# Performance work log

Hardware: AMD Instinct MI355X
Metric: run time of the kernel (lower is better)

Reference implementation:

```python
import jax, jax.numpy as jnp
import numpy as np

N, C, H, W = 2, 32, 56, 56   # batch, in_channels, spatial
O = 64                        # out_channels
PAD = 1                       # ConstantPad2d padding


def _shift(a, dh, dw):
    """Zero-padded shift: out[..., i, j] = a[..., i+dh, j+dw] (out of range -> 0)."""
    nd = a.ndim
    if dh:
        a = jnp.pad(a[..., dh:, :], [(0, 0)] * (nd - 2) + [(0, dh), (0, 0)])
    if dw:
        a = jnp.pad(a[..., :, dw:], [(0, 0)] * (nd - 2) + [(0, 0), (0, dw)])
    return a


def setup_inputs() -> dict:
    key = jax.random.key(0)
    k1, k2, k3 = jax.random.split(key, 3)
    x = jax.random.normal(k1, (N, C, H, W), dtype=jnp.float32)
    # weight entries are used as divisors in extract_param_p; keep them bounded
    # away from zero (magnitude in [0.5, 1.5], random sign) for a stable baseline.
    mag = jax.random.uniform(k2, (O, C, 3, 3), minval=0.5, maxval=1.5, dtype=jnp.float32)
    sgn = jnp.where(jax.random.bernoulli(k3, 0.5, (O, C, 3, 3)), 1.0, -1.0).astype(jnp.float32)
    return {"x": x, "weight": mag * sgn}


def reference(x, weight):
    w = weight  # [O, C, 3, 3]
    # --- extract predict filter P = [p0, p1, p2, p3], each [O, C] ---
    p0 = -w[:, :, 2, 0] / w[:, :, 2, 1]
    p1 = -w[:, :, 0, 2] / w[:, :, 1, 2]
    p2 = (1.0 - w[:, :, 0, 0]
          + w[:, :, 2, 0] * w[:, :, 0, 1] / w[:, :, 2, 1]
          + w[:, :, 0, 2] * w[:, :, 1, 0] / w[:, :, 1, 2]) / w[:, :, 1, 1]
    p3 = -w[:, :, 2, 2] / w[:, :, 1, 1]
    # --- extract update filter U = [u0..u4], each [O, C] ---
    u0, u1, u2, u3, u4 = (w[:, :, 0, 1], w[:, :, 2, 1],
                          w[:, :, 1, 0], w[:, :, 1, 2], w[:, :, 1, 1])

    def bc(c):  # [O, C] -> broadcastable over [N, O, C, Hp, Wp]
        return c[None, :, :, None, None]

    # forward: ConstantPad2d then vanilla lifting scheme (aux_index = 2).
    xp = jnp.pad(x, ((0, 0), (0, 0), (PAD, PAD), (PAD, PAD)))  # [N, C, Hp, Wp]
    x5 = xp[:, None, :, :, :]                                  # [N, 1, C, Hp, Wp]

    x0 = x5
    x1 = _shift(x5, 0, 1)
    x2 = _shift(x5, 1, 0)
    x3 = _shift(x5, 1, 1)
    x0_2 = _shift(x5, 2, 2)

    # predict steps (broadcast to [N, O, C, Hp, Wp])
    x1 = x1 - bc(p0) * x0
    x2 = x2 - bc(p1) * x0
    x3 = x3 - bc(p2) * x0 - bc(p3) * x0_2

    x1_2 = _shift(x1, 2, 0)
    x2_2 = _shift(x2, 0, 2)

    # update steps
    out = (x0
           + bc(u0) * x1 + bc(u1) * x1_2
           + bc(u2) * x2 + bc(u3) * x2_2
           + bc(u4) * x3)

    # crop aux_index=2 border, then sum over in_channels (channel_split loop
    # processes contiguous O slices and concatenates -> identical to full O).
    return out[:, :, :, :-2, :-2].sum(axis=2)  # [N, O, H, W]
```

## Files before the change

### kernel.cpp

```cpp
#include <hip/hip_runtime.h>


namespace {
constexpr int Nn = 2, Cc = 32, Hh = 56, Ww = 56, Oo = 64;

__global__ __launch_bounds__(256)
void lifting_conv_kernel(const float* __restrict__ x,
                         const float* __restrict__ w,
                         float* __restrict__ out)
{
    __shared__ float xs[Cc * 4 * 60];
    __shared__ float ws[8 * Cc * 12];

    const int tid = threadIdx.x;
    const int og  = blockIdx.x;
    const int ip  = blockIdx.y;
    const int n   = blockIdx.z;
    const int i0  = ip * 2;
    const int o0  = og * 8;

    for (int e = tid; e < Cc * 4 * 58; e += 256) {
        const int c   = e / (4 * 58);
        const int rem = e - c * (4 * 58);
        const int r   = rem / 58;
        const int jj  = rem - r * 58;
        const int h   = i0 - 1 + r;
        const int ws_ = jj - 1;
        float v = 0.0f;
        if ((unsigned)h < (unsigned)Hh && (unsigned)ws_ < (unsigned)Ww)
            v = x[((n * Cc + c) * Hh + h) * Ww + ws_];
        xs[(c * 4 + r) * 60 + jj] = v;
    }
    for (int e = tid; e < 8 * Cc * 9; e += 256) {
        const int o   = e / (Cc * 9);
        const int rem = e - o * (Cc * 9);
        const int c   = rem / 9;
        const int k   = rem - c * 9;
        ws[(o * Cc + c) * 12 + k] = w[((o0 + o) * Cc + c) * 9 + k];
    }
    __syncthreads();

    const int lane = tid & 63;
    const int wv   = tid >> 6;
    if (lane >= 56) return;
    const int rsub = (lane >= 28) ? 1 : 0;
    const int cp   = lane - rsub * 28;
    const int col0 = cp * 2;

    float a00 = 0.f, a01 = 0.f, a10 = 0.f, a11 = 0.f;
    const float* xbase = &xs[rsub * 60 + col0];
    const float* wb0   = &ws[(wv * 2 + 0) * (Cc * 12)];
    const float* wb1   = &ws[(wv * 2 + 1) * (Cc * 12)];

    #pragma unroll 4
    for (int c = 0; c < Cc; ++c) {
        const float* xr = xbase + c * 240;
        const float2 r0a = *(const float2*)(xr);
        const float2 r0b = *(const float2*)(xr + 2);
        const float2 r1a = *(const float2*)(xr + 60);
        const float2 r1b = *(const float2*)(xr + 62);
        const float2 r2a = *(const float2*)(xr + 120);
        const float2 r2b = *(const float2*)(xr + 122);

        const float4 wA0 = *(const float4*)(wb0 + c * 12);
        const float4 wB0 = *(const float4*)(wb0 + c * 12 + 4);
        const float  wC0 = wb0[c * 12 + 8];
        a00 += wA0.x * r0a.x + wA0.y * r0a.y + wA0.z * r0b.x
             + wA0.w * r1a.x + wB0.x * r1a.y + wB0.y * r1b.x
             + wB0.z * r2a.x + wB0.w * r2a.y + wC0  * r2b.x;
        a01 += wA0.x * r0a.y + wA0.y * r0b.x + wA0.z * r0b.y
             + wA0.w * r1a.y + wB0.x * r1b.x + wB0.y * r1b.y
             + wB0.z * r2a.y + wB0.w * r2b.x + wC0  * r2b.y;

        const float4 wA1 = *(const float4*)(wb1 + c * 12);
        const float4 wB1 = *(const float4*)(wb1 + c * 12 + 4);
        const float  wC1 = wb1[c * 12 + 8];
        a10 += wA1.x * r0a.x + wA1.y * r0a.y + wA1.z * r0b.x
             + wA1.w * r1a.x + wB1.x * r1a.y + wB1.y * r1b.x
             + wB1.z * r2a.x + wB1.w * r2a.y + wC1  * r2b.x;
        a11 += wA1.x * r0a.y + wA1.y * r0b.x + wA1.z * r0b.y
             + wA1.w * r1a.y + wB1.x * r1b.x + wB1.y * r1b.y
             + wB1.z * r2a.y + wB1.w * r2b.x + wC1  * r2b.y;
    }

    const int row = i0 + rsub;
    const int ob0 = ((n * Oo + o0 + wv * 2 + 0) * Hh + row) * Ww + col0;
    const int ob1 = ob0 + Hh * Ww;
    float2 v0; v0.x = a00; v0.y = a01;
    float2 v1; v1.x = a10; v1.y = a11;
    *(float2*)(out + ob0) = v0;
    *(float2*)(out + ob1) = v1;
}
}

extern "C" void kernel_launch(void* const* d_in, const int* in_sizes, int n_in,
                              void* d_out, int out_size, void* d_ws, size_t ws_size,
                              hipStream_t stream)
{
    const float* x = (const float*)d_in[0];
    const float* w = (const float*)d_in[1];
    float* out = (float*)d_out;

    dim3 grid(8, 28, 2);
    lifting_conv_kernel<<<grid, 256, 0, stream>>>(x, w, out);
}
```

Measured before the change: 76.47 us.

## Read weights as wave-uniform scalar loads and compute four outputs per thread

Drops the shared-memory weight staging and reads weights straight from global memory through a wave-uniform base (readfirstlane), so they can go through scalar loads. Each wave now computes 4 output channels instead of 2, which halves the grid and doubles the reuse of each staged input tile. In exchange there are fewer blocks (224 versus 448) to spread across CUs, and more scalar-load latency in the channel loop.

After: 74.33 us. 1.03x faster.

```diff
diff --git a/kernel.cpp b/kernel.cpp
--- a/kernel.cpp
+++ b/kernel.cpp
@@ -2,7 +2,7 @@
 
 
 namespace {
-constexpr int Nn = 2, Cc = 32, Hh = 56, Ww = 56, Oo = 64;
+constexpr int Cc = 32, Hh = 56, Ww = 56, Oo = 64;
 
 __global__ __launch_bounds__(256)
 void lifting_conv_kernel(const float* __restrict__ x,
@@ -10,14 +10,12 @@
                          float* __restrict__ out)
 {
     __shared__ float xs[Cc * 4 * 60];
-    __shared__ float ws[8 * Cc * 12];
 
     const int tid = threadIdx.x;
     const int og  = blockIdx.x;
     const int ip  = blockIdx.y;
     const int n   = blockIdx.z;
     const int i0  = ip * 2;
-    const int o0  = og * 8;
 
     for (int e = tid; e < Cc * 4 * 58; e += 256) {
         const int c   = e / (4 * 58);
@@ -25,18 +23,11 @@
         const int r   = rem / 58;
         const int jj  = rem - r * 58;
         const int h   = i0 - 1 + r;
-        const int ws_ = jj - 1;
+        const int col = jj - 1;
         float v = 0.0f;
-        if ((unsigned)h < (unsigned)Hh && (unsigned)ws_ < (unsigned)Ww)
-            v = x[((n * Cc + c) * Hh + h) * Ww + ws_];
+        if ((unsigned)h < (unsigned)Hh && (unsigned)col < (unsigned)Ww)
+            v = x[((n * Cc + c) * Hh + h) * Ww + col];
         xs[(c * 4 + r) * 60 + jj] = v;
-    }
-    for (int e = tid; e < 8 * Cc * 9; e += 256) {
-        const int o   = e / (Cc * 9);
-        const int rem = e - o * (Cc * 9);
-        const int c   = rem / 9;
-        const int k   = rem - c * 9;
-        ws[(o * Cc + c) * 12 + k] = w[((o0 + o) * Cc + c) * 9 + k];
     }
     __syncthreads();
 
@@ -47,12 +38,16 @@
     const int cp   = lane - rsub * 28;
     const int col0 = cp * 2;
 
-    float a00 = 0.f, a01 = 0.f, a10 = 0.f, a11 = 0.f;
+    const int o_base = __builtin_amdgcn_readfirstlane(og * 16 + wv * 4);
+    const float* __restrict__ wb = w + (size_t)o_base * Cc * 9;
+
+    float acc[4][2];
+    #pragma unroll
+    for (int i = 0; i < 4; ++i) { acc[i][0] = 0.f; acc[i][1] = 0.f; }
+
     const float* xbase = &xs[rsub * 60 + col0];
-    const float* wb0   = &ws[(wv * 2 + 0) * (Cc * 12)];
-    const float* wb1   = &ws[(wv * 2 + 1) * (Cc * 12)];
 
-    #pragma unroll 4
+    #pragma unroll 2
     for (int c = 0; c < Cc; ++c) {
         const float* xr = xbase + c * 240;
         const float2 r0a = *(const float2*)(xr);
@@ -62,34 +57,27 @@
         const float2 r2a = *(const float2*)(xr + 120);
         const float2 r2b = *(const float2*)(xr + 122);
 
-        const float4 wA0 = *(const float4*)(wb0 + c * 12);
-        const float4 wB0 = *(const float4*)(wb0 + c * 12 + 4);
-        const float  wC0 = wb0[c * 12 + 8];
-        a00 += wA0.x * r0a.x + wA0.y * r0a.y + wA0.z * r0b.x
-             + wA0.w * r1a.x + wB0.x * r1a.y + wB0.y * r1b.x
-             + wB0.z * r2a.x + wB0.w * r2a.y + wC0  * r2b.x;
-        a01 += wA0.x * r0a.y + wA0.y * r0b.x + wA0.z * r0b.y
-             + wA0.w * r1a.y + wB0.x * r1b.x + wB0.y * r1b.y
-             + wB0.z * r2a.y + wB0.w * r2b.x + wC0  * r2b.y;
-
-        const float4 wA1 = *(const float4*)(wb1 + c * 12);
-        const float4 wB1 = *(const float4*)(wb1 + c * 12 + 4);
-        const float  wC1 = wb1[c * 12 + 8];
-        a10 += wA1.x * r0a.x + wA1.y * r0a.y + wA1.z * r0b.x
-             + wA1.w * r1a.x + wB1.x * r1a.y + wB1.y * r1b.x
-             + wB1.z * r2a.x + wB1.w * r2a.y + wC1  * r2b.x;
-        a11 += wA1.x * r0a.y + wA1.y * r0b.x + wA1.z * r0b.y
-             + wA1.w * r1a.y + wB1.x * r1b.x + wB1.y * r1b.y
-             + wB1.z * r2a.y + wB1.w * r2b.x + wC1  * r2b.y;
+        #pragma unroll
+        for (int oo = 0; oo < 4; ++oo) {
+            const float* wc = wb + (oo * Cc + c) * 9;
+            const float w0 = wc[0], w1 = wc[1], w2 = wc[2],
+                        w3 = wc[3], w4 = wc[4], w5 = wc[5],
+                        w6 = wc[6], w7 = wc[7], w8 = wc[8];
+            acc[oo][0] += w0 * r0a.x + w1 * r0a.y + w2 * r0b.x
+                        + w3 * r1a.x + w4 * r1a.y + w5 * r1b.x
+                        + w6 * r2a.x + w7 * r2a.y + w8 * r2b.x;
+            acc[oo][1] += w0 * r0a.y + w1 * r0b.x + w2 * r0b.y
+                        + w3 * r1a.y + w4 * r1b.x + w5 * r1b.y
+                        + w6 * r2a.y + w7 * r2b.x + w8 * r2b.y;
+        }
     }
 
     const int row = i0 + rsub;
-    const int ob0 = ((n * Oo + o0 + wv * 2 + 0) * Hh + row) * Ww + col0;
-    const int ob1 = ob0 + Hh * Ww;
-    float2 v0; v0.x = a00; v0.y = a01;
-    float2 v1; v1.x = a10; v1.y = a11;
-    *(float2*)(out + ob0) = v0;
-    *(float2*)(out + ob1) = v1;
+    #pragma unroll
+    for (int oo = 0; oo < 4; ++oo) {
+        float2 v; v.x = acc[oo][0]; v.y = acc[oo][1];
+        *(float2*)(out + ((size_t)(n * Oo + o_base + oo) * Hh + row) * Ww + col0) = v;
+    }
 }
 }
 
@@ -101,6 +89,6 @@
     const float* w = (const float*)d_in[1];
     float* out = (float*)d_out;
 
-    dim3 grid(8, 28, 2);
+    dim3 grid(4, 28, 2);
     lifting_conv_kernel<<<grid, 256, 0, stream>>>(x, w, out);
 }
```
